# Kernel tuning notes

Measured on AMD Instinct MI355X. Metric: run time of the kernel, lower is better.

The kernel has to match this reference:

```python
import jax, jax.numpy as jnp
import numpy as np

BN_EPS = 1e-5

def setup_inputs() -> dict:
    key = jax.random.key(0)
    ks = jax.random.split(key, 6)
    B, C, N = 8, 256, 4096
    da = C // 4
    return {
        "x": jax.random.normal(ks[0], (B, C, N), dtype=jnp.float32),
        "Wq": jax.random.normal(ks[1], (da, C), dtype=jnp.float32) * (C ** -0.5),
        "Wk": jax.random.normal(ks[2], (da, C), dtype=jnp.float32) * (C ** -0.5),
        "Wv": jax.random.normal(ks[3], (C, C), dtype=jnp.float32) * (C ** -0.5),
        "Wp": jax.random.normal(ks[4], (C, C), dtype=jnp.float32) * (C ** -0.5),
        "bn_gamma": jnp.ones((C,), dtype=jnp.float32),
        "bn_beta": jnp.zeros((C,), dtype=jnp.float32),
        "bn_mean": jnp.zeros((C,), dtype=jnp.float32),
        "bn_var": jnp.ones((C,), dtype=jnp.float32),
    }

def reference(x, Wq, Wk, Wv, Wp, bn_gamma, bn_beta, bn_mean, bn_var):
    # x: [B, C, N]; 1x1 Conv1d == channel matmul
    q = jnp.einsum('bcn,dc->bnd', x, Wq)          # [B, N, da]
    k = jnp.einsum('bcn,dc->bdn', x, Wk)          # [B, da, N]
    v = jnp.einsum('bcn,dc->bnd', x, Wv)          # [B, N, C]
    energy = jnp.einsum('bnd,bdm->bnm', q, k)     # [B, N, N]
    # offset-attention double normalization: softmax over dim=1 (rows), then L1 over dim=-1
    attn = jax.nn.softmax(energy, axis=1)
    attn = attn / (1e-9 + attn.sum(axis=-1, keepdims=True))
    fsa = jnp.einsum('bnm,bmc->bcn', attn, v)     # [B, C, N]
    y = x - fsa
    h = jnp.einsum('bcn,dc->bdn', y, Wp)          # 1x1 conv of LBR
    # BatchNorm1d (inference-mode with running stats)
    inv = bn_gamma / jnp.sqrt(bn_var + BN_EPS)
    h = h * inv[None, :, None] + (bn_beta - bn_mean * inv)[None, :, None]
    return jax.nn.relu(h) + x
```

## Files before the change

kernel.cpp:

```cpp
#include <hip/hip_runtime.h>
#include <math.h>

#define BD 8
#define CD 256
#define ND 4096
#define DA 64
#define CT 272

typedef __attribute__((ext_vector_type(8))) short short8v;
typedef __attribute__((ext_vector_type(4))) float float4v;

static __device__ __forceinline__ float4v mfma16(short8v a, short8v b, float4v c) {
  return __builtin_amdgcn_mfma_f32_16x16x32_bf16(a, b, c, 0, 0, 0);
}
static __device__ __forceinline__ unsigned short f2bf(float f) {
  union { float f; unsigned int u; } v; v.f = f;
  return (unsigned short)((v.u + 0x7fffu + ((v.u >> 16) & 1u)) >> 16);
}
static __device__ __forceinline__ float bf2f(unsigned short h) {
  union { unsigned int u; float f; } v; v.u = (unsigned int)h << 16;
  return v.f;
}
static __device__ __forceinline__ int sw(int row, int c8) {
  return row * 64 + (((c8) ^ (row & 7)) << 3);
}

__global__ __launch_bounds__(256) void k_prep(const float* __restrict__ x,
                                              unsigned short* __restrict__ xTh,
                                              unsigned short* __restrict__ xTl) {
  const int n0 = blockIdx.x * 64, c0 = blockIdx.y * 64, b = blockIdx.z;
  __shared__ float Xs[64][68];
  const int tid = threadIdx.x;
  const int r0 = tid >> 4, col4 = (tid & 15) * 4;
#pragma unroll
  for (int j = 0; j < 4; ++j) {
    int r = r0 + j * 16;
    *(float4*)&Xs[r][col4] =
        *(const float4*)&x[((size_t)(b * CD + c0 + r)) * ND + n0 + col4];
  }
  __syncthreads();
  const int n = tid >> 2, cg = (tid & 3) * 16;
  unsigned short h[16], l[16];
#pragma unroll
  for (int j = 0; j < 16; ++j) {
    float v = Xs[cg + j][n];
    h[j] = f2bf(v);
    l[j] = f2bf(v - bf2f(h[j]));
  }
  size_t o = ((size_t)b * ND + n0 + n) * CD + c0 + cg;
#pragma unroll
  for (int j = 0; j < 4; ++j) {
    *(ushort4*)&xTh[o + j * 4] = *(ushort4*)&h[j * 4];
    *(ushort4*)&xTl[o + j * 4] = *(ushort4*)&l[j * 4];
  }
}

__global__ void k_prepW(const float* __restrict__ Wq, const float* __restrict__ Wk,
                        const float* __restrict__ Wv, const float* __restrict__ Wp,
                        unsigned short* Wqh, unsigned short* Wql,
                        unsigned short* Wkh, unsigned short* Wkl,
                        unsigned short* Wvh, unsigned short* Wvl,
                        unsigned short* Wph, unsigned short* Wpl) {
  int i = blockIdx.x * 256 + threadIdx.x;
  int row = i >> 6, c4 = (i & 63) * 4;
  const float* src; unsigned short *dh, *dl; int r;
  if (row < 64)       { src = Wq; dh = Wqh; dl = Wql; r = row; }
  else if (row < 128) { src = Wk; dh = Wkh; dl = Wkl; r = row - 64; }
  else if (row < 384) { src = Wv; dh = Wvh; dl = Wvl; r = row - 128; }
  else                { src = Wp; dh = Wph; dl = Wpl; r = row - 384; }
  float4 f = *(const float4*)&src[(size_t)r * 256 + c4];
  ushort4 hh, ll;
  hh.x = f2bf(f.x); hh.y = f2bf(f.y); hh.z = f2bf(f.z); hh.w = f2bf(f.w);
  ll.x = f2bf(f.x - bf2f(hh.x)); ll.y = f2bf(f.y - bf2f(hh.y));
  ll.z = f2bf(f.z - bf2f(hh.z)); ll.w = f2bf(f.w - bf2f(hh.w));
  *(ushort4*)&dh[(size_t)r * 256 + c4] = hh;
  *(ushort4*)&dl[(size_t)r * 256 + c4] = ll;
}

__global__ __launch_bounds__(256, 4) void k_proj64(
    const unsigned short* __restrict__ xTh, const unsigned short* __restrict__ xTl,
    const unsigned short* __restrict__ Wh, const unsigned short* __restrict__ Wl,
    unsigned short* __restrict__ oh, unsigned short* __restrict__ ol) {
  const int n0 = blockIdx.x * 128, b = blockIdx.y;
  const int tid = threadIdx.x, w = tid >> 6, lane = tid & 63, lq = lane & 15,
            quad = lane >> 4;
  const int nh = w & 1, dh = w >> 1;
  float4v O[2][4];
#pragma unroll
  for (int dt = 0; dt < 2; ++dt)
#pragma unroll
    for (int nt = 0; nt < 4; ++nt) O[dt][nt] = (float4v){0.f, 0.f, 0.f, 0.f};
#pragma unroll 2
  for (int ks = 0; ks < 8; ++ks) {
    short8v awh[2], awl[2], bxh[4], bxl[4];
#pragma unroll
    for (int dt = 0; dt < 2; ++dt) {
      size_t a = (size_t)(dh * 32 + dt * 16 + lq) * CD + ks * 32 + quad * 8;
      awh[dt] = *(const short8v*)(Wh + a);
      awl[dt] = *(const short8v*)(Wl + a);
    }
#pragma unroll
    for (int nt = 0; nt < 4; ++nt) {
      size_t a = ((size_t)b * ND + n0 + nh * 64 + nt * 16 + lq) * CD + ks * 32 + quad * 8;
      bxh[nt] = *(const short8v*)(xTh + a);
      bxl[nt] = *(const short8v*)(xTl + a);
    }
#pragma unroll
    for (int dt = 0; dt < 2; ++dt)
#pragma unroll
      for (int nt = 0; nt < 4; ++nt) {
        O[dt][nt] = mfma16(awh[dt], bxh[nt], O[dt][nt]);
        O[dt][nt] = mfma16(awl[dt], bxh[nt], O[dt][nt]);
        O[dt][nt] = mfma16(awh[dt], bxl[nt], O[dt][nt]);
      }
  }
#pragma unroll
  for (int dt = 0; dt < 2; ++dt)
#pragma unroll
    for (int nt = 0; nt < 4; ++nt) {
      int d0v = dh * 32 + dt * 16 + quad * 4;
      int n = n0 + nh * 64 + nt * 16 + lq;
      ushort4 hh, ll;
      float v0 = O[dt][nt][0], v1 = O[dt][nt][1], v2 = O[dt][nt][2], v3 = O[dt][nt][3];
      hh.x = f2bf(v0); hh.y = f2bf(v1); hh.z = f2bf(v2); hh.w = f2bf(v3);
      ll.x = f2bf(v0 - bf2f(hh.x)); ll.y = f2bf(v1 - bf2f(hh.y));
      ll.z = f2bf(v2 - bf2f(hh.z)); ll.w = f2bf(v3 - bf2f(hh.w));
      size_t o = ((size_t)b * ND + n) * DA + d0v;
      *(ushort4*)&oh[o] = hh;
      *(ushort4*)&ol[o] = ll;
    }
}

__global__ __launch_bounds__(256, 4) void k_projvT(
    const unsigned short* __restrict__ xTh, const unsigned short* __restrict__ xTl,
    const unsigned short* __restrict__ Wvh, const unsigned short* __restrict__ Wvl,
    unsigned short* __restrict__ vT) {
  const int m0 = blockIdx.x * 128, cob = blockIdx.y * 64, b = blockIdx.z;
  const int tid = threadIdx.x, w = tid >> 6, lane = tid & 63, lq = lane & 15,
            quad = lane >> 4;
  const int mh = w & 1, ch2 = w >> 1;
  float4v O[2][4];
#pragma unroll
  for (int ct = 0; ct < 2; ++ct)
#pragma unroll
    for (int mt = 0; mt < 4; ++mt) O[ct][mt] = (float4v){0.f, 0.f, 0.f, 0.f};
#pragma unroll 2
  for (int ks = 0; ks < 8; ++ks) {
    short8v awh[2], awl[2], bxh[4], bxl[4];
#pragma unroll
    for (int ct = 0; ct < 2; ++ct) {
      size_t a = (size_t)(cob + ch2 * 32 + ct * 16 + lq) * CD + ks * 32 + quad * 8;
      awh[ct] = *(const short8v*)(Wvh + a);
      awl[ct] = *(const short8v*)(Wvl + a);
    }
#pragma unroll
    for (int mt = 0; mt < 4; ++mt) {
      size_t a = ((size_t)b * ND + m0 + mh * 64 + mt * 16 + lq) * CD + ks * 32 + quad * 8;
      bxh[mt] = *(const short8v*)(xTh + a);
      bxl[mt] = *(const short8v*)(xTl + a);
    }
#pragma unroll
    for (int ct = 0; ct < 2; ++ct)
#pragma unroll
      for (int mt = 0; mt < 4; ++mt) {
        O[ct][mt] = mfma16(awh[ct], bxh[mt], O[ct][mt]);
        O[ct][mt] = mfma16(awl[ct], bxh[mt], O[ct][mt]);
        O[ct][mt] = mfma16(awh[ct], bxl[mt], O[ct][mt]);
      }
  }
#pragma unroll
  for (int ct = 0; ct < 2; ++ct)
#pragma unroll
    for (int mt = 0; mt < 4; ++mt) {
      int m = m0 + mh * 64 + mt * 16 + lq;
#pragma unroll
      for (int r = 0; r < 4; ++r) {
        int co = cob + ch2 * 32 + ct * 16 + quad * 4 + r;
        vT[((size_t)b * CT + co) * ND + m] = f2bf(O[ct][mt][r]);
      }
    }
}

__global__ void k_fill(unsigned short* __restrict__ vT) {
  int i = blockIdx.x * 256 + threadIdx.x;
  int b = i >> 14, r = (i >> 10) & 15, n4 = i & 1023;
  unsigned short val = (r == 0) ? (unsigned short)0x3F80 : (unsigned short)0;
  ushort4 v; v.x = val; v.y = val; v.z = val; v.w = val;
  *(ushort4*)&vT[((size_t)b * CT + 256 + r) * ND + n4 * 4] = v;
}

__global__ __launch_bounds__(512, 2) void k_colsum(
    const unsigned short* __restrict__ qh, const unsigned short* __restrict__ ql,
    const unsigned short* __restrict__ kh, const unsigned short* __restrict__ kl,
    float* __restrict__ Drec) {
  const int bid = blockIdx.x, b = bid & 7, m0 = (bid >> 3) * 128;
  const int tid = threadIdx.x, w = tid >> 6, lane = tid & 63, lq = lane & 15,
            quad = lane >> 4;
  const int mq = w & 3, nh = w >> 2;
  __shared__ __align__(16) unsigned short qbuf[2][128 * 64];
  __shared__ float Cb[128];
  short8v bkh[2][2], bkl[2][2];
#pragma unroll
  for (int sub = 0; sub < 2; ++sub)
#pragma unroll
    for (int k = 0; k < 2; ++k) {
      size_t a = ((size_t)b * ND + m0 + mq * 32 + sub * 16 + lq) * DA + k * 32 + quad * 8;
      bkh[sub][k] = *(const short8v*)(kh + a);
      bkl[sub][k] = *(const short8v*)(kl + a);
    }
  uint4 sreg[2];
  const int srow = tid >> 3, sc8 = tid & 7;
  auto load_stage = [&](int nb) {
    sreg[0] = *(const uint4*)(qh + ((size_t)b * ND + nb + srow) * DA + sc8 * 8);
    sreg[1] = *(const uint4*)(ql + ((size_t)b * ND + nb + srow) * DA + sc8 * 8);
  };
  auto write_stage = [&](int buf) {
    *(uint4*)&qbuf[buf][sw(srow, sc8)] = sreg[0];
    *(uint4*)&qbuf[buf][sw(64 + srow, sc8)] = sreg[1];
  };
  load_stage(0); write_stage(0); load_stage(64);
  __syncthreads();
  float cs0 = 0.f, cs1 = 0.f;
  for (int i = 0; i < 64; ++i) {
    const int cur = i & 1;
#pragma unroll
    for (int s = 0; s < 2; ++s) {
      short8v ah[2], al[2];
#pragma unroll
      for (int k = 0; k < 2; ++k) {
        ah[k] = *(const short8v*)&qbuf[cur][sw(nh * 32 + s * 16 + lq, k * 4 + quad)];
        al[k] = *(const short8v*)&qbuf[cur][sw(64 + nh * 32 + s * 16 + lq, k * 4 + quad)];
      }
#pragma unroll
      for (int sub = 0; sub < 2; ++sub) {
        float4v acc = {0.f, 0.f, 0.f, 0.f};
#pragma unroll
        for (int k = 0; k < 2; ++k) {
          acc = mfma16(ah[k], bkh[sub][k], acc);
          acc = mfma16(al[k], bkh[sub][k], acc);
          acc = mfma16(ah[k], bkl[sub][k], acc);
        }
        float e0 = __expf(acc[0]) + __expf(acc[1]) + __expf(acc[2]) + __expf(acc[3]);
        if (sub == 0) cs0 += e0; else cs1 += e0;
      }
    }
    if (i < 63) { write_stage(1 - cur); if (i < 62) load_stage((i + 2) * 64); }
    __syncthreads();
  }
  cs0 += __shfl_down(cs0, 16); cs0 += __shfl_down(cs0, 32);
  cs1 += __shfl_down(cs1, 16); cs1 += __shfl_down(cs1, 32);
  if (nh == 0 && lane < 16) {
    Cb[mq * 32 + lane] = cs0;
    Cb[mq * 32 + 16 + lane] = cs1;
  }
  __syncthreads();
  if (nh == 1 && lane < 16) {
    float t0 = Cb[mq * 32 + lane] + cs0;
    float t1 = Cb[mq * 32 + 16 + lane] + cs1;
    Drec[(size_t)b * ND + m0 + mq * 32 + lane] = 1.0f / t0;
    Drec[(size_t)b * ND + m0 + mq * 32 + 16 + lane] = 1.0f / t1;
  }
}

__global__ __launch_bounds__(512, 2) void k_attn(
    const unsigned short* __restrict__ qh, const unsigned short* __restrict__ ql,
    const unsigned short* __restrict__ kh, const unsigned short* __restrict__ kl,
    const unsigned short* __restrict__ vT, const float* __restrict__ Drec,
    const float* __restrict__ x, unsigned short* __restrict__ y) {
  const int bid = blockIdx.x, b = bid & 7, n0 = (bid >> 3) * 128;
  const int tid = threadIdx.x, w = tid >> 6, lane = tid & 63, lq = lane & 15,
            quad = lane >> 4;
  const int nq = w & 3, ch = w >> 2;
  __shared__ __align__(16) unsigned short kbuf[2][128 * 64];
  __shared__ __align__(16) unsigned short vbuf[2][CT * 64];
  __shared__ __align__(16) unsigned short Pb[128 * 64];
  __shared__ float DrecS[ND];
  __shared__ float Sb[128];
  for (int i = tid; i < ND / 4; i += 512)
    *(float4*)&DrecS[i * 4] = *(const float4*)&Drec[(size_t)b * ND + i * 4];
  short8v aq[2][2][2];
#pragma unroll
  for (int s = 0; s < 2; ++s)
#pragma unroll
    for (int k = 0; k < 2; ++k) {
      size_t a = ((size_t)b * ND + n0 + nq * 32 + s * 16 + lq) * DA + k * 32 + quad * 8;
      aq[s][k][0] = *(const short8v*)(qh + a);
      aq[s][k][1] = *(const short8v*)(ql + a);
    }
  float4v O[2][9];
#pragma unroll
  for (int s = 0; s < 2; ++s)
#pragma unroll
    for (int t = 0; t < 9; ++t) O[s][t] = (float4v){0.f, 0.f, 0.f, 0.f};

  uint4 sk0, sk1, sv[5];
  const int srow = tid >> 3, sc8 = tid & 7;
  auto load_stage = [&](int mb) {
    sk0 = *(const uint4*)(kh + ((size_t)b * ND + mb + srow) * DA + sc8 * 8);
    sk1 = *(const uint4*)(kl + ((size_t)b * ND + mb + srow) * DA + sc8 * 8);
#pragma unroll
    for (int j = 0; j < 4; ++j) {
      int c = tid + j * 512;
      sv[j] = *(const uint4*)(vT + ((size_t)b * CT + (c >> 3)) * ND + mb + (c & 7) * 8);
    }
    if (tid < 128) {
      int c = 2048 + tid;
      sv[4] = *(const uint4*)(vT + ((size_t)b * CT + (c >> 3)) * ND + mb + (c & 7) * 8);
    }
  };
  auto write_stage = [&](int buf) {
    *(uint4*)&kbuf[buf][sw(srow, sc8)] = sk0;
    *(uint4*)&kbuf[buf][sw(64 + srow, sc8)] = sk1;
#pragma unroll
    for (int j = 0; j < 4; ++j) {
      int c = tid + j * 512;
      *(uint4*)&vbuf[buf][sw(c >> 3, c & 7)] = sv[j];
    }
    if (tid < 128) {
      int c = 2048 + tid;
      *(uint4*)&vbuf[buf][sw(c >> 3, c & 7)] = sv[4];
    }
  };
  load_stage(0); write_stage(0); load_stage(64);
  __syncthreads();

#pragma unroll 1
  for (int i = 0; i < 64; ++i) {
    const int cur = i & 1, m0 = i * 64;
#pragma unroll
    for (int sub = 0; sub < 2; ++sub) {
      short8v bh[2], bl[2];
#pragma unroll
      for (int k = 0; k < 2; ++k) {
        bh[k] = *(const short8v*)&kbuf[cur][sw(ch * 32 + sub * 16 + lq, k * 4 + quad)];
        bl[k] = *(const short8v*)&kbuf[cur][sw(64 + ch * 32 + sub * 16 + lq, k * 4 + quad)];
      }
      const int m_loc = ch * 32 + sub * 16 + lq;
      const float dr = DrecS[m0 + m_loc];
#pragma unroll
      for (int s = 0; s < 2; ++s) {
        float4v acc = {0.f, 0.f, 0.f, 0.f};
#pragma unroll
        for (int k = 0; k < 2; ++k) {
          acc = mfma16(aq[s][k][0], bh[k], acc);
          acc = mfma16(aq[s][k][1], bh[k], acc);
          acc = mfma16(aq[s][k][0], bl[k], acc);
        }
        const int nrow = nq * 32 + s * 16 + quad * 4;
#pragma unroll
        for (int r = 0; r < 4; ++r) {
          float p = __expf(acc[r]) * dr;
          const int n_loc = nrow + r;
          Pb[n_loc * 64 + ((((m_loc >> 3) ^ (n_loc & 7)) << 3) | (m_loc & 7))] = f2bf(p);
        }
      }
    }
    if (i < 63) { write_stage(1 - cur); if (i < 62) load_stage((i + 2) * 64); }
    __syncthreads();
    short8v ap[2][2];
#pragma unroll
    for (int s = 0; s < 2; ++s)
#pragma unroll
      for (int k = 0; k < 2; ++k)
        ap[s][k] = *(const short8v*)&Pb[sw(nq * 32 + s * 16 + lq, k * 4 + quad)];
    const int tbase = ch * 9;
#pragma unroll
    for (int ti = 0; ti < 8; ++ti) {
      const int t = tbase + ti;
#pragma unroll
      for (int k = 0; k < 2; ++k) {
        short8v bv = *(const short8v*)&vbuf[cur][sw(t * 16 + lq, k * 4 + quad)];
#pragma unroll
        for (int s = 0; s < 2; ++s) O[s][ti] = mfma16(ap[s][k], bv, O[s][ti]);
      }
    }
    if (ch == 0) {
#pragma unroll
      for (int k = 0; k < 2; ++k) {
        short8v bv = *(const short8v*)&vbuf[cur][sw(8 * 16 + lq, k * 4 + quad)];
#pragma unroll
        for (int s = 0; s < 2; ++s) O[s][8] = mfma16(ap[s][k], bv, O[s][8]);
      }
    }
    __syncthreads();
  }
  if (ch == 1 && lq == 0) {
#pragma unroll
    for (int s = 0; s < 2; ++s)
#pragma unroll
      for (int r = 0; r < 4; ++r)
        Sb[nq * 32 + s * 16 + quad * 4 + r] = O[s][7][r];
  }
  __syncthreads();
  float rsc[2][4];
#pragma unroll
  for (int s = 0; s < 2; ++s)
#pragma unroll
    for (int r = 0; r < 4; ++r)
      rsc[s][r] = 1.0f / (1e-9f + Sb[nq * 32 + s * 16 + quad * 4 + r]);
#pragma unroll
  for (int ti = 0; ti < 9; ++ti) {
    const bool active = (ch == 0) || (ti < 7);
    if (active) {
      const int c = (ch * 9 + ti) * 16 + lq;
#pragma unroll
      for (int s = 0; s < 2; ++s)
#pragma unroll
        for (int r = 0; r < 4; ++r) {
          const int n = n0 + nq * 32 + s * 16 + quad * 4 + r;
          float xv = x[((size_t)(b * CD + c)) * ND + n];
          y[((size_t)b * ND + n) * CD + c] = f2bf(xv - O[s][ti][r] * rsc[s][r]);
        }
    }
  }
}

__global__ __launch_bounds__(256) void k_final(const unsigned short* __restrict__ y,
                                               const unsigned short* __restrict__ Wpb,
                                               const float* __restrict__ x,
                                               const float* __restrict__ gamma,
                                               const float* __restrict__ beta,
                                               const float* __restrict__ mean,
                                               const float* __restrict__ var,
                                               float* __restrict__ out) {
  const int bid = blockIdx.x;
  const int b = bid & 7;
  const int rem = bid >> 3;
  const int n0 = (rem & 63) * 64;
  const int d0 = (rem >> 6) * 64;
  const int tid = threadIdx.x;
  const int wave = tid >> 6, lane = tid & 63, lq = lane & 15, quad = lane >> 4;
  const int dw = d0 + wave * 16;
  float4v O[4];
#pragma unroll
  for (int s = 0; s < 4; ++s) O[s] = (float4v){0.f, 0.f, 0.f, 0.f};
#pragma unroll
  for (int chh = 0; chh < 8; ++chh) {
    const size_t ab = (size_t)(dw + lq) * CD + chh * 32 + quad * 8;
    short8v a0 = *(const short8v*)(Wpb + ab);
#pragma unroll
    for (int s = 0; s < 4; ++s) {
      const size_t bb = ((size_t)b * ND + n0 + s * 16 + lq) * CD + chh * 32 + quad * 8;
      short8v bv = *(const short8v*)(y + bb);
      O[s] = mfma16(a0, bv, O[s]);
    }
  }
#pragma unroll
  for (int r = 0; r < 4; ++r) {
    const int d = dw + quad * 4 + r;
    const float inv  = gamma[d] / sqrtf(var[d] + 1e-5f);
    const float bias = beta[d] - mean[d] * inv;
#pragma unroll
    for (int s = 0; s < 4; ++s) {
      const int n = n0 + s * 16 + lq;
      const size_t oi = ((size_t)b * CD + d) * ND + n;
      out[oi] = fmaxf(O[s][r] * inv + bias, 0.f) + x[oi];
    }
  }
}

extern "C" void kernel_launch(void* const* d_in, const int* in_sizes, int n_in,
                              void* d_out, int out_size, void* d_ws, size_t ws_size,
                              hipStream_t stream) {
  const float* x     = (const float*)d_in[0];
  const float* Wq    = (const float*)d_in[1];
  const float* Wk    = (const float*)d_in[2];
  const float* Wv    = (const float*)d_in[3];
  const float* Wp    = (const float*)d_in[4];
  const float* gamma = (const float*)d_in[5];
  const float* beta  = (const float*)d_in[6];
  const float* mean  = (const float*)d_in[7];
  const float* var   = (const float*)d_in[8];
  float* out = (float*)d_out;

  char* wsp = (char*)d_ws;
  unsigned short* qh  = (unsigned short*)wsp; wsp += (size_t)BD * ND * DA * 2;
  unsigned short* ql  = (unsigned short*)wsp; wsp += (size_t)BD * ND * DA * 2;
  unsigned short* khp = (unsigned short*)wsp; wsp += (size_t)BD * ND * DA * 2;
  unsigned short* klp = (unsigned short*)wsp; wsp += (size_t)BD * ND * DA * 2;
  unsigned short* vT  = (unsigned short*)wsp; wsp += (size_t)BD * CT * ND * 2;
  unsigned short* xTh = (unsigned short*)wsp; wsp += (size_t)BD * ND * CD * 2;
  unsigned short* xTl = (unsigned short*)wsp; wsp += (size_t)BD * ND * CD * 2;
  unsigned short* Wqh = (unsigned short*)wsp; wsp += (size_t)64 * 256 * 2;
  unsigned short* Wql = (unsigned short*)wsp; wsp += (size_t)64 * 256 * 2;
  unsigned short* Wkh = (unsigned short*)wsp; wsp += (size_t)64 * 256 * 2;
  unsigned short* Wkl = (unsigned short*)wsp; wsp += (size_t)64 * 256 * 2;
  unsigned short* Wvh = (unsigned short*)wsp; wsp += (size_t)256 * 256 * 2;
  unsigned short* Wvl = (unsigned short*)wsp; wsp += (size_t)256 * 256 * 2;
  unsigned short* Wph = (unsigned short*)wsp; wsp += (size_t)256 * 256 * 2;
  unsigned short* Wpl = (unsigned short*)wsp; wsp += (size_t)256 * 256 * 2;
  float* Drec = (float*)wsp; wsp += (size_t)BD * ND * 4;
  unsigned short* y = xTh;

  dim3 blk(256), blk5(512);
  k_prep<<<dim3(ND / 64, CD / 64, BD), blk, 0, stream>>>(x, xTh, xTl);
  k_prepW<<<dim3(160), blk, 0, stream>>>(Wq, Wk, Wv, Wp, Wqh, Wql, Wkh, Wkl,
                                         Wvh, Wvl, Wph, Wpl);
  k_proj64<<<dim3(ND / 128, BD), blk, 0, stream>>>(xTh, xTl, Wqh, Wql, qh, ql);
  k_proj64<<<dim3(ND / 128, BD), blk, 0, stream>>>(xTh, xTl, Wkh, Wkl, khp, klp);
  k_projvT<<<dim3(ND / 128, 4, BD), blk, 0, stream>>>(xTh, xTl, Wvh, Wvl, vT);
  k_fill<<<dim3(512), blk, 0, stream>>>(vT);
  k_colsum<<<dim3(256), blk5, 0, stream>>>(qh, ql, khp, klp, Drec);
  k_attn<<<dim3(256), blk5, 0, stream>>>(qh, ql, khp, klp, vT, Drec, x, y);
  k_final<<<dim3(2048), blk, 0, stream>>>(y, Wph, x, gamma, beta, mean, var, out);
}
```

Baseline: 532.6 us.

## Split colsum over N halves, async LDS V staging, register K in attention

k_colsum now splits the N reduction into two halves, doubling the grid and raising the occupancy hint; a new k_rcp kernel adds the partial sums and takes the reciprocal. k_attn stages V with global_load_lds into a triple buffer, double-buffers P so one barrier per iteration is enough, and loads K fragments straight into registers with prefetch. The P conversion truncates instead of rounding to nearest. The epilogue rebuilds x from the bf16 hi/lo split with vectorized loads and writes y in place, replacing strided fp32 x reads. The cost is one extra kernel launch, more register pressure, and slightly lower precision for x and P.

Result: faster. 519.9 us (-2.4%).

```diff
diff --git a/kernel.cpp b/kernel.cpp
--- a/kernel.cpp
+++ b/kernel.cpp
@@ -23,6 +23,11 @@
 }
 static __device__ __forceinline__ int sw(int row, int c8) {
   return row * 64 + (((c8) ^ (row & 7)) << 3);
+}
+typedef const __attribute__((address_space(1))) unsigned int g_u32;
+typedef __attribute__((address_space(3))) unsigned int l_u32;
+static __device__ __forceinline__ void gld16(const void* g, void* l) {
+  __builtin_amdgcn_global_load_lds((g_u32*)g, (l_u32*)l, 16, 0, 0);
 }
 
 __global__ __launch_bounds__(256) void k_prep(const float* __restrict__ x,
@@ -189,11 +194,13 @@
   *(ushort4*)&vT[((size_t)b * CT + 256 + r) * ND + n4 * 4] = v;
 }
 
-__global__ __launch_bounds__(512, 2) void k_colsum(
+__global__ __launch_bounds__(512, 4) void k_colsum(
     const unsigned short* __restrict__ qh, const unsigned short* __restrict__ ql,
     const unsigned short* __restrict__ kh, const unsigned short* __restrict__ kl,
-    float* __restrict__ Drec) {
-  const int bid = blockIdx.x, b = bid & 7, m0 = (bid >> 3) * 128;
+    float* __restrict__ Dp) {
+  const int bid = blockIdx.x, b = bid & 7, half = (bid >> 3) & 1,
+            m0 = (bid >> 4) * 128;
+  const int nbase = half * 2048;
   const int tid = threadIdx.x, w = tid >> 6, lane = tid & 63, lq = lane & 15,
             quad = lane >> 4;
   const int mq = w & 3, nh = w >> 2;
@@ -218,10 +225,10 @@
     *(uint4*)&qbuf[buf][sw(srow, sc8)] = sreg[0];
     *(uint4*)&qbuf[buf][sw(64 + srow, sc8)] = sreg[1];
   };
-  load_stage(0); write_stage(0); load_stage(64);
+  load_stage(nbase); write_stage(0); load_stage(nbase + 64);
   __syncthreads();
   float cs0 = 0.f, cs1 = 0.f;
-  for (int i = 0; i < 64; ++i) {
+  for (int i = 0; i < 32; ++i) {
     const int cur = i & 1;
 #pragma unroll
     for (int s = 0; s < 2; ++s) {
@@ -244,7 +251,7 @@
         if (sub == 0) cs0 += e0; else cs1 += e0;
       }
     }
-    if (i < 63) { write_stage(1 - cur); if (i < 62) load_stage((i + 2) * 64); }
+    if (i < 31) { write_stage(1 - cur); if (i < 30) load_stage(nbase + (i + 2) * 64); }
     __syncthreads();
   }
   cs0 += __shfl_down(cs0, 16); cs0 += __shfl_down(cs0, 32);
@@ -257,27 +264,36 @@
   if (nh == 1 && lane < 16) {
     float t0 = Cb[mq * 32 + lane] + cs0;
     float t1 = Cb[mq * 32 + 16 + lane] + cs1;
-    Drec[(size_t)b * ND + m0 + mq * 32 + lane] = 1.0f / t0;
-    Drec[(size_t)b * ND + m0 + mq * 32 + 16 + lane] = 1.0f / t1;
-  }
+    size_t o = (size_t)half * (BD * ND) + (size_t)b * ND + m0 + mq * 32 + lane;
+    Dp[o] = t0;
+    Dp[o + 16] = t1;
+  }
+}
+
+__global__ void k_rcp(const float* __restrict__ Dp, float* __restrict__ Drec) {
+  int i = blockIdx.x * 256 + threadIdx.x;
+  float4 a = *(const float4*)&Dp[(size_t)i * 4];
+  float4 c = *(const float4*)&Dp[(size_t)(BD * ND) + (size_t)i * 4];
+  float4 r;
+  r.x = 1.f / (a.x + c.x); r.y = 1.f / (a.y + c.y);
+  r.z = 1.f / (a.z + c.z); r.w = 1.f / (a.w + c.w);
+  *(float4*)&Drec[(size_t)i * 4] = r;
 }
 
 __global__ __launch_bounds__(512, 2) void k_attn(
     const unsigned short* __restrict__ qh, const unsigned short* __restrict__ ql,
-    const unsigned short* __restrict__ kh, const unsigned short* __restrict__ kl,
+    const unsigned short* __restrict__ khp, const unsigned short* __restrict__ klp,
     const unsigned short* __restrict__ vT, const float* __restrict__ Drec,
-    const float* __restrict__ x, unsigned short* __restrict__ y) {
+    unsigned short* xhy, const unsigned short* __restrict__ xTl) {
   const int bid = blockIdx.x, b = bid & 7, n0 = (bid >> 3) * 128;
   const int tid = threadIdx.x, w = tid >> 6, lane = tid & 63, lq = lane & 15,
             quad = lane >> 4;
   const int nq = w & 3, ch = w >> 2;
-  __shared__ __align__(16) unsigned short kbuf[2][128 * 64];
-  __shared__ __align__(16) unsigned short vbuf[2][CT * 64];
-  __shared__ __align__(16) unsigned short Pb[128 * 64];
+  __shared__ __align__(16) unsigned short vbuf[3][CT * 64];
+  __shared__ __align__(16) unsigned short Pb[2][128 * 64];
   __shared__ float DrecS[ND];
   __shared__ float Sb[128];
-  for (int i = tid; i < ND / 4; i += 512)
-    *(float4*)&DrecS[i * 4] = *(const float4*)&Drec[(size_t)b * ND + i * 4];
+
   short8v aq[2][2][2];
 #pragma unroll
   for (int s = 0; s < 2; ++s)
@@ -293,124 +309,128 @@
 #pragma unroll
     for (int t = 0; t < 9; ++t) O[s][t] = (float4v){0.f, 0.f, 0.f, 0.f};
 
-  uint4 sk0, sk1, sv[5];
-  const int srow = tid >> 3, sc8 = tid & 7;
-  auto load_stage = [&](int mb) {
-    sk0 = *(const uint4*)(kh + ((size_t)b * ND + mb + srow) * DA + sc8 * 8);
-    sk1 = *(const uint4*)(kl + ((size_t)b * ND + mb + srow) * DA + sc8 * 8);
+  auto stageV = [&](int mt, int vn) {
+    unsigned short* base = &vbuf[vn][0];
 #pragma unroll
     for (int j = 0; j < 4; ++j) {
-      int c = tid + j * 512;
-      sv[j] = *(const uint4*)(vT + ((size_t)b * CT + (c >> 3)) * ND + mb + (c & 7) * 8);
+      int cidx = tid + j * 512;
+      int row = cidx >> 3, ckpos = cidx & 7;
+      const unsigned short* src =
+          vT + ((size_t)b * CT + row) * ND + mt * 64 + ((ckpos ^ (row & 7)) << 3);
+      gld16(src, base + (size_t)(w * 64 + j * 512) * 8);
     }
     if (tid < 128) {
-      int c = 2048 + tid;
-      sv[4] = *(const uint4*)(vT + ((size_t)b * CT + (c >> 3)) * ND + mb + (c & 7) * 8);
+      int cidx = 2048 + tid;
+      int row = cidx >> 3, ckpos = cidx & 7;
+      const unsigned short* src =
+          vT + ((size_t)b * CT + row) * ND + mt * 64 + ((ckpos ^ (row & 7)) << 3);
+      gld16(src, base + (size_t)(2048 + w * 64) * 8);
     }
   };
-  auto write_stage = [&](int buf) {
-    *(uint4*)&kbuf[buf][sw(srow, sc8)] = sk0;
-    *(uint4*)&kbuf[buf][sw(64 + srow, sc8)] = sk1;
-#pragma unroll
-    for (int j = 0; j < 4; ++j) {
-      int c = tid + j * 512;
-      *(uint4*)&vbuf[buf][sw(c >> 3, c & 7)] = sv[j];
-    }
-    if (tid < 128) {
-      int c = 2048 + tid;
-      *(uint4*)&vbuf[buf][sw(c >> 3, c & 7)] = sv[4];
-    }
+  short8v kc[8], kn[8];
+  auto kload = [&](short8v* dst, int mt) {
+#pragma unroll
+    for (int sub = 0; sub < 2; ++sub)
+#pragma unroll
+      for (int k = 0; k < 2; ++k) {
+        size_t a = ((size_t)b * ND + mt * 64 + ch * 32 + sub * 16 + lq) * DA +
+                   k * 32 + quad * 8;
+        dst[sub * 4 + k * 2 + 0] = *(const short8v*)(khp + a);
+        dst[sub * 4 + k * 2 + 1] = *(const short8v*)(klp + a);
+      }
   };
-  load_stage(0); write_stage(0); load_stage(64);
+
+  stageV(0, 0);
+  kload(kc, 0);
+  for (int idx = tid; idx < ND / 4; idx += 512)
+    *(float4*)&DrecS[idx * 4] = *(const float4*)&Drec[(size_t)b * ND + idx * 4];
   __syncthreads();
 
+  int vn = 0;
 #pragma unroll 1
   for (int i = 0; i < 64; ++i) {
-    const int cur = i & 1, m0 = i * 64;
+    int vnext = vn + 1; if (vnext == 3) vnext = 0;
+    if (i < 63) { stageV(i + 1, vnext); kload(kn, i + 1); }
+    unsigned short* Pcur = &Pb[i & 1][0];
 #pragma unroll
     for (int sub = 0; sub < 2; ++sub) {
-      short8v bh[2], bl[2];
-#pragma unroll
-      for (int k = 0; k < 2; ++k) {
-        bh[k] = *(const short8v*)&kbuf[cur][sw(ch * 32 + sub * 16 + lq, k * 4 + quad)];
-        bl[k] = *(const short8v*)&kbuf[cur][sw(64 + ch * 32 + sub * 16 + lq, k * 4 + quad)];
-      }
       const int m_loc = ch * 32 + sub * 16 + lq;
-      const float dr = DrecS[m0 + m_loc];
+      const float dr = DrecS[(i << 6) + m_loc];
 #pragma unroll
       for (int s = 0; s < 2; ++s) {
         float4v acc = {0.f, 0.f, 0.f, 0.f};
 #pragma unroll
         for (int k = 0; k < 2; ++k) {
-          acc = mfma16(aq[s][k][0], bh[k], acc);
-          acc = mfma16(aq[s][k][1], bh[k], acc);
-          acc = mfma16(aq[s][k][0], bl[k], acc);
+          acc = mfma16(aq[s][k][0], kc[sub * 4 + k * 2 + 0], acc);
+          acc = mfma16(aq[s][k][1], kc[sub * 4 + k * 2 + 0], acc);
+          acc = mfma16(aq[s][k][0], kc[sub * 4 + k * 2 + 1], acc);
         }
         const int nrow = nq * 32 + s * 16 + quad * 4;
 #pragma unroll
         for (int r = 0; r < 4; ++r) {
           float p = __expf(acc[r]) * dr;
           const int n_loc = nrow + r;
-          Pb[n_loc * 64 + ((((m_loc >> 3) ^ (n_loc & 7)) << 3) | (m_loc & 7))] = f2bf(p);
+          union { float f; unsigned int u; } pu; pu.f = p;
+          Pcur[n_loc * 64 + ((((m_loc >> 3) ^ (n_loc & 7)) << 3) | (m_loc & 7))] =
+              (unsigned short)(pu.u >> 16);
         }
       }
     }
-    if (i < 63) { write_stage(1 - cur); if (i < 62) load_stage((i + 2) * 64); }
     __syncthreads();
+    const unsigned short* Pc = &Pb[i & 1][0];
+    const unsigned short* vc = &vbuf[vn][0];
     short8v ap[2][2];
 #pragma unroll
     for (int s = 0; s < 2; ++s)
 #pragma unroll
       for (int k = 0; k < 2; ++k)
-        ap[s][k] = *(const short8v*)&Pb[sw(nq * 32 + s * 16 + lq, k * 4 + quad)];
-    const int tbase = ch * 9;
-#pragma unroll
-    for (int ti = 0; ti < 8; ++ti) {
-      const int t = tbase + ti;
-#pragma unroll
-      for (int k = 0; k < 2; ++k) {
-        short8v bv = *(const short8v*)&vbuf[cur][sw(t * 16 + lq, k * 4 + quad)];
-#pragma unroll
-        for (int s = 0; s < 2; ++s) O[s][ti] = mfma16(ap[s][k], bv, O[s][ti]);
-      }
-    }
-    if (ch == 0) {
-#pragma unroll
-      for (int k = 0; k < 2; ++k) {
-        short8v bv = *(const short8v*)&vbuf[cur][sw(8 * 16 + lq, k * 4 + quad)];
-#pragma unroll
-        for (int s = 0; s < 2; ++s) O[s][8] = mfma16(ap[s][k], bv, O[s][8]);
-      }
-    }
-    __syncthreads();
-  }
-  if (ch == 1 && lq == 0) {
-#pragma unroll
-    for (int s = 0; s < 2; ++s)
-#pragma unroll
-      for (int r = 0; r < 4; ++r)
-        Sb[nq * 32 + s * 16 + quad * 4 + r] = O[s][7][r];
+        ap[s][k] = *(const short8v*)&Pc[sw(nq * 32 + s * 16 + lq, k * 4 + quad)];
+#pragma unroll
+    for (int ti = 0; ti < 9; ++ti) {
+      if (ch == 0 || ti < 8) {
+        const int t = ch * 9 + ti;
+#pragma unroll
+        for (int k = 0; k < 2; ++k) {
+          short8v bv = *(const short8v*)&vc[sw(t * 16 + lq, k * 4 + quad)];
+#pragma unroll
+          for (int s = 0; s < 2; ++s) O[s][ti] = mfma16(bv, ap[s][k], O[s][ti]);
+        }
+      }
+    }
+    if (i < 63) {
+#pragma unroll
+      for (int t = 0; t < 8; ++t) kc[t] = kn[t];
+    }
+    vn = vnext;
+  }
+  if (ch == 1 && quad == 0) {
+#pragma unroll
+    for (int s = 0; s < 2; ++s) Sb[nq * 32 + s * 16 + lq] = O[s][7][0];
   }
   __syncthreads();
-  float rsc[2][4];
+  float rsc[2];
 #pragma unroll
   for (int s = 0; s < 2; ++s)
-#pragma unroll
-    for (int r = 0; r < 4; ++r)
-      rsc[s][r] = 1.0f / (1e-9f + Sb[nq * 32 + s * 16 + quad * 4 + r]);
+    rsc[s] = 1.0f / (1e-9f + Sb[nq * 32 + s * 16 + lq]);
 #pragma unroll
   for (int ti = 0; ti < 9; ++ti) {
     const bool active = (ch == 0) || (ti < 7);
     if (active) {
-      const int c = (ch * 9 + ti) * 16 + lq;
-#pragma unroll
-      for (int s = 0; s < 2; ++s)
-#pragma unroll
-        for (int r = 0; r < 4; ++r) {
-          const int n = n0 + nq * 32 + s * 16 + quad * 4 + r;
-          float xv = x[((size_t)(b * CD + c)) * ND + n];
-          y[((size_t)b * ND + n) * CD + c] = f2bf(xv - O[s][ti][r] * rsc[s][r]);
-        }
+      const int t = ch * 9 + ti;
+      const int cb = t * 16 + quad * 4;
+#pragma unroll
+      for (int s = 0; s < 2; ++s) {
+        const int n = n0 + nq * 32 + s * 16 + lq;
+        const size_t off = ((size_t)b * ND + n) * CD + cb;
+        ushort4 h4 = *(const ushort4*)&xhy[off];
+        ushort4 l4 = *(const ushort4*)&xTl[off];
+        ushort4 o4;
+        o4.x = f2bf(bf2f(h4.x) + bf2f(l4.x) - O[s][ti][0] * rsc[s]);
+        o4.y = f2bf(bf2f(h4.y) + bf2f(l4.y) - O[s][ti][1] * rsc[s]);
+        o4.z = f2bf(bf2f(h4.z) + bf2f(l4.z) - O[s][ti][2] * rsc[s]);
+        o4.w = f2bf(bf2f(h4.w) + bf2f(l4.w) - O[s][ti][3] * rsc[s]);
+        *(ushort4*)&xhy[off] = o4;
+      }
     }
   }
 }
@@ -490,6 +510,7 @@
   unsigned short* Wph = (unsigned short*)wsp; wsp += (size_t)256 * 256 * 2;
   unsigned short* Wpl = (unsigned short*)wsp; wsp += (size_t)256 * 256 * 2;
   float* Drec = (float*)wsp; wsp += (size_t)BD * ND * 4;
+  float* Dp   = (float*)wsp; wsp += (size_t)2 * BD * ND * 4;
   unsigned short* y = xTh;
 
   dim3 blk(256), blk5(512);
@@ -500,7 +521,8 @@
   k_proj64<<<dim3(ND / 128, BD), blk, 0, stream>>>(xTh, xTl, Wkh, Wkl, khp, klp);
   k_projvT<<<dim3(ND / 128, 4, BD), blk, 0, stream>>>(xTh, xTl, Wvh, Wvl, vT);
   k_fill<<<dim3(512), blk, 0, stream>>>(vT);
-  k_colsum<<<dim3(256), blk5, 0, stream>>>(qh, ql, khp, klp, Drec);
-  k_attn<<<dim3(256), blk5, 0, stream>>>(qh, ql, khp, klp, vT, Drec, x, y);
+  k_colsum<<<dim3(512), blk5, 0, stream>>>(qh, ql, khp, klp, Dp);
+  k_rcp<<<dim3(32), blk, 0, stream>>>(Dp, Drec);
+  k_attn<<<dim3(256), blk5, 0, stream>>>(qh, ql, khp, klp, vT, Drec, y, xTl);
   k_final<<<dim3(2048), blk, 0, stream>>>(y, Wph, x, gamma, beta, mean, var, out);
 }
```
